# Optimization experiments

Measured on AMD Instinct MI355X. Metric: run time of the kernel, lower is better.

Reference implementation:

```python
import jax, jax.numpy as jnp
import numpy as np

RES_SCALE = 0.1
B, C, H, W = 16, 256, 96, 96


def conv3x3(x, w):
    # NCHW input, OIHW weight, SAME padding (padding=1 for k=3), no bias
    return jax.lax.conv_general_dilated(
        x, w, window_strides=(1, 1), padding="SAME",
        dimension_numbers=("NCHW", "OIHW", "NCHW"))


def setup_inputs() -> dict:
    key = jax.random.key(0)
    k1, k2, k3, k4 = jax.random.split(key, 4)
    fan = C * 9
    x = jax.random.normal(k1, (B, C, H, W), dtype=jnp.float32)
    conv2_w = jax.random.normal(k2, (C, C, 3, 3), dtype=jnp.float32) / np.sqrt(fan)
    conv3_w = jax.random.normal(k3, (C, C, 3, 3), dtype=jnp.float32) / np.sqrt(fan)
    prelu_w = jnp.full((1,), 0.25, dtype=jnp.float32)  # nn.PReLU default init
    # interleaved channel partition: P=0::3 (86), R=1::3 (85), T=2::3 (85)
    idx_p = jnp.arange(0, C, 3, dtype=jnp.int32)
    idx_r = jnp.arange(1, C, 3, dtype=jnp.int32)
    idx_t = jnp.arange(2, C, 3, dtype=jnp.int32)
    return {"x": x, "conv2_w": conv2_w, "conv3_w": conv3_w, "prelu_w": prelu_w,
            "idx_p": idx_p, "idx_r": idx_r, "idx_t": idx_t}


def reference(x, conv2_w, conv3_w, prelu_w, idx_p, idx_r, idx_t):
    # op2 = conv2(prune(x, skip_gate)) ; all-ones gate -> identity prune
    op2 = conv3x3(x, conv2_w)  # [B, C, H, W]
    # per-channel activation routing (gathers permute channel order to [P,R,T])
    gp = op2[:, idx_p]                                  # [B, 86, H, W]
    a = jnp.concatenate([
        jnp.where(gp >= 0, gp, prelu_w[0] * gp),        # PReLU (1 shared param)
        jax.nn.relu(op2[:, idx_r]),                     # [B, 85, H, W]
        jnp.tanh(op2[:, idx_t]),                        # [B, 85, H, W]
    ], axis=1)                                          # [B, C, H, W]
    # conv_tot branch: op3 = conv3(a)*res_scale + x * reshape(skip_conv_gate)
    # skip_conv_gate == ones here, so the skip scaling is identity
    op3 = conv3x3(a, conv3_w) * RES_SCALE + x
    return op3


if __name__ == "__main__":
    out = reference(**setup_inputs())
    print(out.shape, out.dtype)
```

## Files before the change

### kernel.cpp

```cpp
#include <hip/hip_runtime.h>
#include <math.h>


#define Bn 16
#define Cn 256
#define Hn 96
#define Wn 96
#define PH 98
#define PW 98
#define HW (Hn*Wn)

typedef __bf16 bf16x8 __attribute__((ext_vector_type(8)));
typedef float  f32x4  __attribute__((ext_vector_type(4)));

__device__ __forceinline__ unsigned short f2bf(float f) {
    unsigned int u = __float_as_uint(f);
    unsigned int r = (u + 0x7fffu + ((u >> 16) & 1u)) >> 16;
    return (unsigned short)r;
}

__device__ __forceinline__ void lds_load16(void* lds, const void* g) {
    auto gp = (const __attribute__((address_space(1))) char*)(unsigned long long)(uintptr_t)g;
    auto lp = (__attribute__((address_space(3))) char*)(unsigned int)(uintptr_t)lds;
    __builtin_amdgcn_global_load_lds(gp, lp, 16, 0, 0);
}

#define SB() __builtin_amdgcn_sched_barrier(0)
#define MEMFENCE() asm volatile("" ::: "memory")

__global__ __launch_bounds__(256)
void zero_border_k(unsigned short* __restrict__ t) {
    int idx = blockIdx.x * 256 + threadIdx.x;
    int oct = idx & 31;
    int rest = idx >> 5;
    int pidx = rest % 388;
    int b = rest / 388;
    int h, w;
    if (pidx < 98)       { h = 0;  w = pidx; }
    else if (pidx < 196) { h = 97; w = pidx - 98; }
    else if (pidx < 292) { h = pidx - 196 + 1; w = 0; }
    else                 { h = pidx - 292 + 1; w = 97; }
    size_t e = ((size_t)(b * PH + h) * PW + w) * 256 + oct * 8;
    *(uint4*)(t + e) = make_uint4(0u, 0u, 0u, 0u);
}

template<bool PERM>
__global__ __launch_bounds__(256)
void pack_w_k(const float* __restrict__ w, unsigned short* __restrict__ wp) {
    int idx = blockIdx.x * 256 + threadIdx.x;
    int ci_l = idx & 31;
    int c    = (idx >> 5) & 255;
    int v    = idx >> 13;
    int k9   = v % 9;
    int cc   = v / 9;
    int co;
    if (PERM) {
        co = (c < 86) ? c * 3 : (c < 171) ? (c - 86) * 3 + 1 : (c - 171) * 3 + 2;
    } else {
        co = c;
    }
    float val = w[((size_t)co * 256 + cc * 32 + ci_l) * 9 + k9];
    wp[idx] = f2bf(val);
}

__global__ __launch_bounds__(256)
void transform_x_k(const float* __restrict__ x, unsigned short* __restrict__ xp) {
    __shared__ float s[32 * 33];
    const int t = threadIdx.x;
    const int col0 = blockIdx.x * 32;
    const int row  = blockIdx.y;
    const int z = blockIdx.z;
    const int b = z >> 3;
    const int ci0 = (z & 7) * 32;

    #pragma unroll
    for (int i = 0; i < 4; ++i) {
        int ci = i * 8 + (t >> 5);
        int px = t & 31;
        s[ci * 33 + px] = x[((size_t)(b * Cn + ci0 + ci)) * HW + row * Wn + col0 + px];
    }
    __syncthreads();
    const int px = t >> 3;
    const int c4 = (t & 7) * 4;
    ushort4 o;
    o.x = f2bf(s[(c4 + 0) * 33 + px]);
    o.y = f2bf(s[(c4 + 1) * 33 + px]);
    o.z = f2bf(s[(c4 + 2) * 33 + px]);
    o.w = f2bf(s[(c4 + 3) * 33 + px]);
    size_t e = ((size_t)(b * PH + row + 1) * PW + (col0 + px + 1)) * 256 + ci0 + c4;
    *(ushort4*)(xp + e) = o;
}

template<int MODE>
__global__ __launch_bounds__(256, 4)
void conv_k(const unsigned short* __restrict__ in_cl,
            const unsigned short* __restrict__ wp,
            const float* __restrict__ prelu_w,
            const float* __restrict__ xres,
            void* __restrict__ outp)
{
    __shared__ unsigned short s_x[1536 * 8];
    __shared__ unsigned short s_w[2][256 * 8];

    const int tid = threadIdx.x;
    const int bid = blockIdx.x;
    const int wg = (bid & 7) * 288 + (bid >> 3);
    const int co_base = (wg & 3) * 64;
    const int t2 = wg >> 2;
    const int tile = t2 % 36;
    const int b = t2 / 36;
    const int R0 = (tile / 3) * 8;
    const int C0 = (tile % 3) * 32;

    const int lane = tid & 63;
    const int wv = tid >> 6;
    const int l15 = lane & 15;
    const int qq = lane >> 4;
    const int qa = qq ^ ((l15 >> 1) & 3);

    const unsigned short* img = in_cl + (size_t)b * PH * PW * 256;

    int xg[6];
    #pragma unroll
    for (int i = 0; i < 6; ++i) {
        int slot = i * 256 + tid;
        int lsl = slot ^ ((slot >> 3) & 3);
        if (lsl > 1359) lsl = 1359;
        int p = lsl >> 2;
        int pr = p / 34, pc = p - pr * 34;
        xg[i] = ((R0 + pr) * PW + (C0 + pc)) * 256 + (lsl & 3) * 8;
    }
    int wroff;
    {
        int lsl = tid ^ ((tid >> 3) & 3);
        wroff = (co_base + (lsl >> 2)) * 32 + (lsl & 3) * 8;
    }

    f32x4 acc[4][4];
    #pragma unroll
    for (int m = 0; m < 4; ++m)
        #pragma unroll
        for (int n = 0; n < 4; ++n) acc[m][n] = 0.f;

    lds_load16(&s_w[0][(size_t)tid * 8], wp + wroff);
    #pragma unroll
    for (int i = 0; i < 6; ++i)
        lds_load16(&s_x[(size_t)(i * 256 + tid) * 8], img + xg[i]);
    MEMFENCE(); SB();
    asm volatile("s_waitcnt vmcnt(0)" ::: "memory");
    SB();
    __builtin_amdgcn_s_barrier();
    SB();

    for (int c = 0; c < 8; ++c) {
        #pragma unroll
        for (int k9 = 0; k9 < 9; ++k9) {
            const int s = c * 9 + k9;
            const int kh = k9 / 3, kw = k9 - 3 * kh;
            const unsigned short* swc = s_w[s & 1];

            if (c < 7 || k9 < 8)
                lds_load16(&s_w[(s + 1) & 1][(size_t)tid * 8],
                           wp + (size_t)(s + 1) * 8192 + wroff);
            MEMFENCE(); SB();

            bf16x8 af[4], bf[4];
            #pragma unroll
            for (int m = 0; m < 4; ++m)
                af[m] = *(const bf16x8*)&swc[(m * 16 + l15) * 32 + qa * 8];
            #pragma unroll
            for (int n = 0; n < 4; ++n) {
                const int P = (wv * 2 + (n >> 1) + kh) * 34 + (n & 1) * 16 + l15 + kw;
                bf[n] = *(const bf16x8*)&s_x[P * 32 + ((qq ^ ((P >> 1) & 3)) << 3)];
            }
            __builtin_amdgcn_s_setprio(1);
            #pragma unroll
            for (int n = 0; n < 4; ++n)
                #pragma unroll
                for (int m = 0; m < 4; ++m)
                    acc[m][n] = __builtin_amdgcn_mfma_f32_16x16x32_bf16(af[m], bf[n], acc[m][n], 0, 0, 0);
            __builtin_amdgcn_s_setprio(0);
            SB();

            if (k9 < 8) {
                asm volatile("s_waitcnt vmcnt(0)" ::: "memory");
                SB();
                __builtin_amdgcn_s_barrier();
                SB();
            }
        }
        __builtin_amdgcn_s_barrier();
        SB();
        if (c < 7) {
            #pragma unroll
            for (int i = 0; i < 6; ++i)
                lds_load16(&s_x[(size_t)(i * 256 + tid) * 8],
                           img + xg[i] + (c + 1) * 32);
            MEMFENCE(); SB();
        }
        asm volatile("s_waitcnt vmcnt(0)" ::: "memory");
        SB();
        __builtin_amdgcn_s_barrier();
        SB();
    }

    if constexpr (MODE == 0) {
        const float pw = prelu_w[0];
        unsigned short* aout = (unsigned short*)outp;
        #pragma unroll
        for (int n = 0; n < 4; ++n) {
            const int row_p = wv * 2 + (n >> 1);
            const int col_p = (n & 1) * 16 + l15;
            size_t pix = ((size_t)(b * PH + R0 + row_p + 1)) * PW + (C0 + col_p + 1);
            #pragma unroll
            for (int m = 0; m < 4; ++m) {
                const int cb = co_base + m * 16 + qq * 4;
                float r[4];
                #pragma unroll
                for (int j = 0; j < 4; ++j) {
                    const int ch = cb + j;
                    float s = acc[m][n][j];
                    if (ch < 86)        r[j] = s >= 0.f ? s : pw * s;
                    else if (ch < 171)  r[j] = fmaxf(s, 0.f);
                    else {
                        float e = __expf(2.f * s);
                        r[j] = 1.f - 2.f / (e + 1.f);
                    }
                }
                ushort4 o;
                o.x = f2bf(r[0]); o.y = f2bf(r[1]); o.z = f2bf(r[2]); o.w = f2bf(r[3]);
                *(ushort4*)(aout + pix * 256 + cb) = o;
            }
        }
    } else {
        float* fout = (float*)outp;
        #pragma unroll
        for (int n = 0; n < 4; ++n) {
            const int row_p = wv * 2 + (n >> 1);
            const int col_p = (n & 1) * 16 + l15;
            #pragma unroll
            for (int m = 0; m < 4; ++m) {
                const int cb = co_base + m * 16 + qq * 4;
                size_t base = ((size_t)(b * Cn + cb)) * HW + (size_t)(R0 + row_p) * Wn + (C0 + col_p);
                #pragma unroll
                for (int j = 0; j < 4; ++j)
                    fout[base + (size_t)j * HW] = acc[m][n][j] * 0.1f + xres[base + (size_t)j * HW];
            }
        }
    }
}

extern "C" void kernel_launch(void* const* d_in, const int* in_sizes, int n_in,
                              void* d_out, int out_size, void* d_ws, size_t ws_size,
                              hipStream_t stream) {
    const float* x  = (const float*)d_in[0];
    const float* w2 = (const float*)d_in[1];
    const float* w3 = (const float*)d_in[2];
    const float* pw = (const float*)d_in[3];
    float* out = (float*)d_out;
    char* ws = (char*)d_ws;

    unsigned short* a_cl = (unsigned short*)ws;
    unsigned short* wp2  = (unsigned short*)(ws + 78675968);
    unsigned short* wp3  = (unsigned short*)(ws + 78675968 + 1179648);
    unsigned short* x_pad = (unsigned short*)d_out;

    zero_border_k<<<776, 256, 0, stream>>>(x_pad);
    zero_border_k<<<776, 256, 0, stream>>>(a_cl);
    pack_w_k<true ><<<2304, 256, 0, stream>>>(w2, wp2);
    pack_w_k<false><<<2304, 256, 0, stream>>>(w3, wp3);
    transform_x_k<<<dim3(3, 96, 128), 256, 0, stream>>>(x, x_pad);

    conv_k<0><<<2304, 256, 0, stream>>>(x_pad, wp2, pw, nullptr, (void*)a_cl);
    conv_k<1><<<2304, 256, 0, stream>>>(a_cl, wp3, nullptr, x, (void*)out);
}
```

Before: 433.8 us.

## Retile conv to full 256 output channels with 32x32x16 MFMA and double-buffered input

After: 482.7 us. 1.11x slower.

```diff
diff --git a/kernel.cpp b/kernel.cpp
--- a/kernel.cpp
+++ b/kernel.cpp
@@ -11,7 +11,7 @@
 #define HW (Hn*Wn)
 
 typedef __bf16 bf16x8 __attribute__((ext_vector_type(8)));
-typedef float  f32x4  __attribute__((ext_vector_type(4)));
+typedef float  f32x16 __attribute__((ext_vector_type(16)));
 
 __device__ __forceinline__ unsigned short f2bf(float f) {
     unsigned int u = __float_as_uint(f);
@@ -92,113 +92,127 @@
 }
 
 template<int MODE>
-__global__ __launch_bounds__(256, 4)
+__global__ __launch_bounds__(256, 2)
 void conv_k(const unsigned short* __restrict__ in_cl,
             const unsigned short* __restrict__ wp,
             const float* __restrict__ prelu_w,
             const float* __restrict__ xres,
             void* __restrict__ outp)
 {
-    __shared__ unsigned short s_x[1536 * 8];
-    __shared__ unsigned short s_w[2][256 * 8];
+    __shared__ unsigned short s_x[2][1024 * 8];
+    __shared__ unsigned short s_w[2][1024 * 8];
 
     const int tid = threadIdx.x;
     const int bid = blockIdx.x;
-    const int wg = (bid & 7) * 288 + (bid >> 3);
-    const int co_base = (wg & 3) * 64;
-    const int t2 = wg >> 2;
-    const int tile = t2 % 36;
-    const int b = t2 / 36;
-    const int R0 = (tile / 3) * 8;
+    const int wg = (bid & 7) * 144 + (bid >> 3);
+    const int tile = wg % 72;
+    const int b = wg / 72;
+    const int R0 = (tile / 3) * 4;
     const int C0 = (tile % 3) * 32;
 
     const int lane = tid & 63;
     const int wv = tid >> 6;
-    const int l15 = lane & 15;
-    const int qq = lane >> 4;
-    const int qa = qq ^ ((l15 >> 1) & 3);
+    const int l31 = lane & 31;
+    const int lh = lane >> 5;
+    const int ch = wv & 1;
+    const int ph = wv >> 1;
+    const int swA = (l31 >> 1) & 3;
 
     const unsigned short* img = in_cl + (size_t)b * PH * PW * 256;
 
-    int xg[6];
-    #pragma unroll
-    for (int i = 0; i < 6; ++i) {
+    int xg[4];
+    #pragma unroll
+    for (int i = 0; i < 4; ++i) {
         int slot = i * 256 + tid;
         int lsl = slot ^ ((slot >> 3) & 3);
-        if (lsl > 1359) lsl = 1359;
+        if (lsl > 815) lsl = 815;
         int p = lsl >> 2;
         int pr = p / 34, pc = p - pr * 34;
         xg[i] = ((R0 + pr) * PW + (C0 + pc)) * 256 + (lsl & 3) * 8;
     }
-    int wroff;
-    {
-        int lsl = tid ^ ((tid >> 3) & 3);
-        wroff = (co_base + (lsl >> 2)) * 32 + (lsl & 3) * 8;
-    }
-
-    f32x4 acc[4][4];
+    int wgo[4];
+    #pragma unroll
+    for (int i = 0; i < 4; ++i) {
+        int slot = i * 256 + tid;
+        int lsl = slot ^ ((slot >> 3) & 3);
+        wgo[i] = (lsl >> 2) * 32 + (lsl & 3) * 8;
+    }
+
+    f32x16 acc[4][2];
     #pragma unroll
     for (int m = 0; m < 4; ++m)
         #pragma unroll
-        for (int n = 0; n < 4; ++n) acc[m][n] = 0.f;
-
-    lds_load16(&s_w[0][(size_t)tid * 8], wp + wroff);
-    #pragma unroll
-    for (int i = 0; i < 6; ++i)
-        lds_load16(&s_x[(size_t)(i * 256 + tid) * 8], img + xg[i]);
+        for (int n = 0; n < 2; ++n) acc[m][n] = 0.f;
+
+    #pragma unroll
+    for (int i = 0; i < 4; ++i) lds_load16(&s_w[0][(size_t)(i * 256 + tid) * 8], wp + wgo[i]);
+    #pragma unroll
+    for (int i = 0; i < 4; ++i) lds_load16(&s_x[0][(size_t)(i * 256 + tid) * 8], img + xg[i]);
     MEMFENCE(); SB();
     asm volatile("s_waitcnt vmcnt(0)" ::: "memory");
     SB();
     __builtin_amdgcn_s_barrier();
     SB();
 
-    for (int c = 0; c < 8; ++c) {
-        #pragma unroll
-        for (int k9 = 0; k9 < 9; ++k9) {
-            const int s = c * 9 + k9;
-            const int kh = k9 / 3, kw = k9 - 3 * kh;
-            const unsigned short* swc = s_w[s & 1];
-
-            if (c < 7 || k9 < 8)
-                lds_load16(&s_w[(s + 1) & 1][(size_t)tid * 8],
-                           wp + (size_t)(s + 1) * 8192 + wroff);
+    for (int s = 0; s < 72; ++s) {
+        const int c  = s / 9;
+        const int k9 = s - 9 * c;
+        const int kh = k9 / 3, kw = k9 - 3 * kh;
+        const unsigned short* swc = s_w[s & 1];
+        const unsigned short* sxc = s_x[c & 1];
+
+        if (s < 71) {
+            #pragma unroll
+            for (int i = 0; i < 4; ++i)
+                lds_load16(&s_w[(s + 1) & 1][(size_t)(i * 256 + tid) * 8],
+                           wp + (size_t)(s + 1) * 8192 + wgo[i]);
             MEMFENCE(); SB();
-
-            bf16x8 af[4], bf[4];
-            #pragma unroll
-            for (int m = 0; m < 4; ++m)
-                af[m] = *(const bf16x8*)&swc[(m * 16 + l15) * 32 + qa * 8];
-            #pragma unroll
-            for (int n = 0; n < 4; ++n) {
-                const int P = (wv * 2 + (n >> 1) + kh) * 34 + (n & 1) * 16 + l15 + kw;
-                bf[n] = *(const bf16x8*)&s_x[P * 32 + ((qq ^ ((P >> 1) & 3)) << 3)];
-            }
-            __builtin_amdgcn_s_setprio(1);
-            #pragma unroll
-            for (int n = 0; n < 4; ++n)
-                #pragma unroll
-                for (int m = 0; m < 4; ++m)
-                    acc[m][n] = __builtin_amdgcn_mfma_f32_16x16x32_bf16(af[m], bf[n], acc[m][n], 0, 0, 0);
-            __builtin_amdgcn_s_setprio(0);
-            SB();
-
-            if (k9 < 8) {
-                asm volatile("s_waitcnt vmcnt(0)" ::: "memory");
-                SB();
-                __builtin_amdgcn_s_barrier();
-                SB();
-            }
-        }
-        __builtin_amdgcn_s_barrier();
-        SB();
-        if (c < 7) {
-            #pragma unroll
-            for (int i = 0; i < 6; ++i)
-                lds_load16(&s_x[(size_t)(i * 256 + tid) * 8],
+        }
+        if (k9 == 8 && c < 7) {
+            #pragma unroll
+            for (int i = 0; i < 4; ++i)
+                lds_load16(&s_x[(c + 1) & 1][(size_t)(i * 256 + tid) * 8],
                            img + xg[i] + (c + 1) * 32);
             MEMFENCE(); SB();
         }
-        asm volatile("s_waitcnt vmcnt(0)" ::: "memory");
+        if (k9 == 0 && c > 0) {
+            asm volatile("s_waitcnt vmcnt(4)" ::: "memory");
+            SB();
+        }
+
+        bf16x8 a0[4], a1[4], b0[2], b1[2];
+        #pragma unroll
+        for (int m = 0; m < 4; ++m) {
+            const int row = ch * 128 + m * 32 + l31;
+            a0[m] = *(const bf16x8*)&swc[(row * 4 + (lh ^ swA)) * 8];
+            a1[m] = *(const bf16x8*)&swc[(row * 4 + ((2 + lh) ^ swA)) * 8];
+        }
+        #pragma unroll
+        for (int n = 0; n < 2; ++n) {
+            const int px = (ph * 2 + n + kh) * 34 + l31 + kw;
+            const int swB = (px >> 1) & 3;
+            b0[n] = *(const bf16x8*)&sxc[(px * 4 + (lh ^ swB)) * 8];
+            b1[n] = *(const bf16x8*)&sxc[(px * 4 + ((2 + lh) ^ swB)) * 8];
+        }
+        __builtin_amdgcn_s_setprio(1);
+        #pragma unroll
+        for (int n = 0; n < 2; ++n)
+            #pragma unroll
+            for (int m = 0; m < 4; ++m)
+                acc[m][n] = __builtin_amdgcn_mfma_f32_32x32x16_bf16(a0[m], b0[n], acc[m][n], 0, 0, 0);
+        #pragma unroll
+        for (int n = 0; n < 2; ++n)
+            #pragma unroll
+            for (int m = 0; m < 4; ++m)
+                acc[m][n] = __builtin_amdgcn_mfma_f32_32x32x16_bf16(a1[m], b1[n], acc[m][n], 0, 0, 0);
+        __builtin_amdgcn_s_setprio(0);
+        SB();
+
+        if (k9 == 8 && c < 7) {
+            asm volatile("s_waitcnt vmcnt(4)" ::: "memory");
+        } else if (s < 71) {
+            asm volatile("s_waitcnt vmcnt(0)" ::: "memory");
+        }
         SB();
         __builtin_amdgcn_s_barrier();
         SB();
@@ -208,43 +222,48 @@
         const float pw = prelu_w[0];
         unsigned short* aout = (unsigned short*)outp;
         #pragma unroll
-        for (int n = 0; n < 4; ++n) {
-            const int row_p = wv * 2 + (n >> 1);
-            const int col_p = (n & 1) * 16 + l15;
-            size_t pix = ((size_t)(b * PH + R0 + row_p + 1)) * PW + (C0 + col_p + 1);
+        for (int n = 0; n < 2; ++n) {
+            const int prow = R0 + ph * 2 + n + 1;
+            size_t pix = ((size_t)(b * PH + prow)) * PW + (C0 + l31 + 1);
             #pragma unroll
             for (int m = 0; m < 4; ++m) {
-                const int cb = co_base + m * 16 + qq * 4;
-                float r[4];
+                const int chb = ch * 128 + m * 32;
                 #pragma unroll
-                for (int j = 0; j < 4; ++j) {
-                    const int ch = cb + j;
-                    float s = acc[m][n][j];
-                    if (ch < 86)        r[j] = s >= 0.f ? s : pw * s;
-                    else if (ch < 171)  r[j] = fmaxf(s, 0.f);
-                    else {
-                        float e = __expf(2.f * s);
-                        r[j] = 1.f - 2.f / (e + 1.f);
+                for (int p = 0; p < 8; ++p) {
+                    const int base = chb + (p & 1) * 2 + (p >> 1) * 8 + 4 * lh;
+                    float v0 = acc[m][n][2 * p];
+                    float v1 = acc[m][n][2 * p + 1];
+                    float r0, r1;
+                    {
+                        const int c0_ = base;
+                        if (c0_ < 86)       r0 = v0 >= 0.f ? v0 : pw * v0;
+                        else if (c0_ < 171) r0 = fmaxf(v0, 0.f);
+                        else { float e = __expf(2.f * v0); r0 = 1.f - 2.f / (e + 1.f); }
+                        const int c1_ = base + 1;
+                        if (c1_ < 86)       r1 = v1 >= 0.f ? v1 : pw * v1;
+                        else if (c1_ < 171) r1 = fmaxf(v1, 0.f);
+                        else { float e = __expf(2.f * v1); r1 = 1.f - 2.f / (e + 1.f); }
                     }
+                    unsigned int u = (unsigned int)f2bf(r0) | ((unsigned int)f2bf(r1) << 16);
+                    *(unsigned int*)(aout + pix * 256 + base) = u;
                 }
-                ushort4 o;
-                o.x = f2bf(r[0]); o.y = f2bf(r[1]); o.z = f2bf(r[2]); o.w = f2bf(r[3]);
-                *(ushort4*)(aout + pix * 256 + cb) = o;
             }
         }
     } else {
         float* fout = (float*)outp;
         #pragma unroll
-        for (int n = 0; n < 4; ++n) {
-            const int row_p = wv * 2 + (n >> 1);
-            const int col_p = (n & 1) * 16 + l15;
+        for (int n = 0; n < 2; ++n) {
+            const int row = R0 + ph * 2 + n;
+            const int col = C0 + l31;
             #pragma unroll
             for (int m = 0; m < 4; ++m) {
-                const int cb = co_base + m * 16 + qq * 4;
-                size_t base = ((size_t)(b * Cn + cb)) * HW + (size_t)(R0 + row_p) * Wn + (C0 + col_p);
+                const int chb = ch * 128 + m * 32;
                 #pragma unroll
-                for (int j = 0; j < 4; ++j)
-                    fout[base + (size_t)j * HW] = acc[m][n][j] * 0.1f + xres[base + (size_t)j * HW];
+                for (int r = 0; r < 16; ++r) {
+                    const int chn = chb + (r & 3) + 8 * (r >> 2) + 4 * lh;
+                    size_t idx = ((size_t)(b * Cn + chn)) * HW + (size_t)row * Wn + col;
+                    fout[idx] = acc[m][n][r] * 0.1f + xres[idx];
+                }
             }
         }
     }
@@ -271,6 +290,6 @@
     pack_w_k<false><<<2304, 256, 0, stream>>>(w3, wp3);
     transform_x_k<<<dim3(3, 96, 128), 256, 0, stream>>>(x, x_pad);
 
-    conv_k<0><<<2304, 256, 0, stream>>>(x_pad, wp2, pw, nullptr, (void*)a_cl);
-    conv_k<1><<<2304, 256, 0, stream>>>(a_cl, wp3, nullptr, x, (void*)out);
-}
+    conv_k<0><<<1152, 256, 0, stream>>>(x_pad, wp2, pw, nullptr, (void*)a_cl);
+    conv_k<1><<<1152, 256, 0, stream>>>(a_cl, wp3, nullptr, x, (void*)out);
+}
```

## Enlarge conv tiles to all 256 output channels with double-buffered input staging

Applied to the files above, without the earlier changes.

New measurement: 1.148 ms. 2.65x slower.

```diff
diff --git a/kernel.cpp b/kernel.cpp
--- a/kernel.cpp
+++ b/kernel.cpp
@@ -92,60 +92,66 @@
 }
 
 template<int MODE>
-__global__ __launch_bounds__(256, 4)
+__global__ __launch_bounds__(512) __attribute__((amdgpu_waves_per_eu(2, 2)))
 void conv_k(const unsigned short* __restrict__ in_cl,
             const unsigned short* __restrict__ wp,
             const float* __restrict__ prelu_w,
             const float* __restrict__ xres,
             void* __restrict__ outp)
 {
-    __shared__ unsigned short s_x[1536 * 8];
-    __shared__ unsigned short s_w[2][256 * 8];
+    __shared__ unsigned short s_a[2][1024 * 8];
+    __shared__ unsigned short s_b[2][2048 * 8];
 
     const int tid = threadIdx.x;
     const int bid = blockIdx.x;
-    const int wg = (bid & 7) * 288 + (bid >> 3);
-    const int co_base = (wg & 3) * 64;
-    const int t2 = wg >> 2;
-    const int tile = t2 % 36;
-    const int b = t2 / 36;
-    const int R0 = (tile / 3) * 8;
-    const int C0 = (tile % 3) * 32;
+    const int wg = (bid & 7) * 64 + (bid >> 3);
+    const int tile = wg % 32;
+    const int b = wg / 32;
+    const int tr = tile >> 1;
+    const int tc = tile & 1;
+    const int R0 = tr * 6;
+    const int C0 = tc * 48;
 
     const int lane = tid & 63;
     const int wv = tid >> 6;
     const int l15 = lane & 15;
     const int qq = lane >> 4;
+    const int g  = wv & 3;
+    const int h  = wv >> 2;
     const int qa = qq ^ ((l15 >> 1) & 3);
 
     const unsigned short* img = in_cl + (size_t)b * PH * PW * 256;
 
-    int xg[6];
-    #pragma unroll
-    for (int i = 0; i < 6; ++i) {
-        int slot = i * 256 + tid;
+    int bxg[4];
+    #pragma unroll
+    for (int i = 0; i < 4; ++i) {
+        int slot = i * 512 + tid;
         int lsl = slot ^ ((slot >> 3) & 3);
-        if (lsl > 1359) lsl = 1359;
+        if (lsl > 1599) lsl = 1599;
         int p = lsl >> 2;
-        int pr = p / 34, pc = p - pr * 34;
-        xg[i] = ((R0 + pr) * PW + (C0 + pc)) * 256 + (lsl & 3) * 8;
-    }
-    int wroff;
-    {
-        int lsl = tid ^ ((tid >> 3) & 3);
-        wroff = (co_base + (lsl >> 2)) * 32 + (lsl & 3) * 8;
-    }
-
-    f32x4 acc[4][4];
+        int pr = p / 50, pc = p - pr * 50;
+        bxg[i] = ((R0 + pr) * PW + (C0 + pc)) * 256 + (lsl & 3) * 8;
+    }
+    int axg[2];
+    #pragma unroll
+    for (int i = 0; i < 2; ++i) {
+        int slot = i * 512 + tid;
+        int lsl = slot ^ ((slot >> 3) & 3);
+        axg[i] = (lsl >> 2) * 32 + (lsl & 3) * 8;
+    }
+
+    f32x4 acc[4][9];
     #pragma unroll
     for (int m = 0; m < 4; ++m)
         #pragma unroll
-        for (int n = 0; n < 4; ++n) acc[m][n] = 0.f;
-
-    lds_load16(&s_w[0][(size_t)tid * 8], wp + wroff);
-    #pragma unroll
-    for (int i = 0; i < 6; ++i)
-        lds_load16(&s_x[(size_t)(i * 256 + tid) * 8], img + xg[i]);
+        for (int n = 0; n < 9; ++n) acc[m][n] = 0.f;
+
+    #pragma unroll
+    for (int i = 0; i < 2; ++i)
+        lds_load16(&s_a[0][(size_t)(i * 512 + tid) * 8], wp + axg[i]);
+    #pragma unroll
+    for (int i = 0; i < 4; ++i)
+        lds_load16(&s_b[0][(size_t)(i * 512 + tid) * 8], img + bxg[i]);
     MEMFENCE(); SB();
     asm volatile("s_waitcnt vmcnt(0)" ::: "memory");
     SB();
@@ -157,64 +163,67 @@
         for (int k9 = 0; k9 < 9; ++k9) {
             const int s = c * 9 + k9;
             const int kh = k9 / 3, kw = k9 - 3 * kh;
-            const unsigned short* swc = s_w[s & 1];
-
-            if (c < 7 || k9 < 8)
-                lds_load16(&s_w[(s + 1) & 1][(size_t)tid * 8],
-                           wp + (size_t)(s + 1) * 8192 + wroff);
+            const unsigned short* sac = s_a[s & 1];
+            const unsigned short* sbc = s_b[c & 1];
+
+            if (s < 71) {
+                #pragma unroll
+                for (int i = 0; i < 2; ++i)
+                    lds_load16(&s_a[(s + 1) & 1][(size_t)(i * 512 + tid) * 8],
+                               wp + (size_t)(s + 1) * 8192 + axg[i]);
+            }
+            if (c < 7 && k9 >= 4 && k9 <= 7) {
+                const int i = k9 - 4;
+                lds_load16(&s_b[(c + 1) & 1][(size_t)(i * 512 + tid) * 8],
+                           img + bxg[i] + (c + 1) * 32);
+            }
             MEMFENCE(); SB();
 
-            bf16x8 af[4], bf[4];
-            #pragma unroll
-            for (int m = 0; m < 4; ++m)
-                af[m] = *(const bf16x8*)&swc[(m * 16 + l15) * 32 + qa * 8];
-            #pragma unroll
-            for (int n = 0; n < 4; ++n) {
-                const int P = (wv * 2 + (n >> 1) + kh) * 34 + (n & 1) * 16 + l15 + kw;
-                bf[n] = *(const bf16x8*)&s_x[P * 32 + ((qq ^ ((P >> 1) & 3)) << 3)];
-            }
+            bf16x8 af[4], bf[9];
+            #pragma unroll
+            for (int m = 0; m < 4; ++m) {
+                const int co = g * 64 + m * 16 + l15;
+                af[m] = *(const bf16x8*)&sac[co * 32 + qa * 8];
+            }
+            #pragma unroll
+            for (int n = 0; n < 9; ++n) {
+                const int hr = h * 9 + n;
+                const int P = (hr / 3 + kh) * 50 + (hr % 3) * 16 + l15 + kw;
+                bf[n] = *(const bf16x8*)&sbc[P * 32 + ((qq ^ ((P >> 1) & 3)) << 3)];
+            }
+            MEMFENCE(); SB();
+            __builtin_amdgcn_s_barrier();
+            asm volatile("s_waitcnt lgkmcnt(0)" ::: "memory");
+            SB();
+
             __builtin_amdgcn_s_setprio(1);
             #pragma unroll
-            for (int n = 0; n < 4; ++n)
+            for (int n = 0; n < 9; ++n)
                 #pragma unroll
                 for (int m = 0; m < 4; ++m)
                     acc[m][n] = __builtin_amdgcn_mfma_f32_16x16x32_bf16(af[m], bf[n], acc[m][n], 0, 0, 0);
             __builtin_amdgcn_s_setprio(0);
             SB();
 
-            if (k9 < 8) {
-                asm volatile("s_waitcnt vmcnt(0)" ::: "memory");
-                SB();
-                __builtin_amdgcn_s_barrier();
-                SB();
-            }
+            asm volatile("s_waitcnt vmcnt(0)" ::: "memory");
+            SB();
+            __builtin_amdgcn_s_barrier();
+            SB();
         }
-        __builtin_amdgcn_s_barrier();
-        SB();
-        if (c < 7) {
-            #pragma unroll
-            for (int i = 0; i < 6; ++i)
-                lds_load16(&s_x[(size_t)(i * 256 + tid) * 8],
-                           img + xg[i] + (c + 1) * 32);
-            MEMFENCE(); SB();
-        }
-        asm volatile("s_waitcnt vmcnt(0)" ::: "memory");
-        SB();
-        __builtin_amdgcn_s_barrier();
-        SB();
     }
 
     if constexpr (MODE == 0) {
         const float pw = prelu_w[0];
         unsigned short* aout = (unsigned short*)outp;
         #pragma unroll
-        for (int n = 0; n < 4; ++n) {
-            const int row_p = wv * 2 + (n >> 1);
-            const int col_p = (n & 1) * 16 + l15;
-            size_t pix = ((size_t)(b * PH + R0 + row_p + 1)) * PW + (C0 + col_p + 1);
+        for (int n = 0; n < 9; ++n) {
+            const int hr = h * 9 + n;
+            const int row_p = R0 + hr / 3 + 1;
+            const int col_p = C0 + (hr % 3) * 16 + l15 + 1;
+            size_t pix = ((size_t)(b * PH + row_p)) * PW + col_p;
             #pragma unroll
             for (int m = 0; m < 4; ++m) {
-                const int cb = co_base + m * 16 + qq * 4;
+                const int cb = g * 64 + m * 16 + qq * 4;
                 float r[4];
                 #pragma unroll
                 for (int j = 0; j < 4; ++j) {
@@ -235,13 +244,14 @@
     } else {
         float* fout = (float*)outp;
         #pragma unroll
-        for (int n = 0; n < 4; ++n) {
-            const int row_p = wv * 2 + (n >> 1);
-            const int col_p = (n & 1) * 16 + l15;
+        for (int n = 0; n < 9; ++n) {
+            const int hr = h * 9 + n;
+            const int row = tr * 6 + hr / 3;
+            const int col = tc * 48 + (hr % 3) * 16 + l15;
             #pragma unroll
             for (int m = 0; m < 4; ++m) {
-                const int cb = co_base + m * 16 + qq * 4;
-                size_t base = ((size_t)(b * Cn + cb)) * HW + (size_t)(R0 + row_p) * Wn + (C0 + col_p);
+                const int cb = g * 64 + m * 16 + qq * 4;
+                size_t base = ((size_t)(b * Cn + cb)) * HW + (size_t)row * Wn + col;
                 #pragma unroll
                 for (int j = 0; j < 4; ++j)
                     fout[base + (size_t)j * HW] = acc[m][n][j] * 0.1f + xres[base + (size_t)j * HW];
@@ -271,6 +281,6 @@
     pack_w_k<false><<<2304, 256, 0, stream>>>(w3, wp3);
     transform_x_k<<<dim3(3, 96, 128), 256, 0, stream>>>(x, x_pad);
 
-    conv_k<0><<<2304, 256, 0, stream>>>(x_pad, wp2, pw, nullptr, (void*)a_cl);
-    conv_k<1><<<2304, 256, 0, stream>>>(a_cl, wp3, nullptr, x, (void*)out);
-}
+    conv_k<0><<<512, 512, 0, stream>>>(x_pad, wp2, pw, nullptr, (void*)a_cl);
+    conv_k<1><<<512, 512, 0, stream>>>(a_cl, wp3, nullptr, x, (void*)out);
+}
```
